# Kernel optimization log

Measured on AMD Instinct MI355X. Metric: run time of the kernel, lower is better.

## Reference

```python
import jax, jax.numpy as jnp
import numpy as np

EMBED_DIM = 1024
HEADS = 16
HEAD_DIM = EMBED_DIM // HEADS


def setup_inputs() -> dict:
    key = jax.random.key(0)
    ks = jax.random.split(key, 5)
    B, N, C = 2, 2048, EMBED_DIM
    scale = 1.0 / np.sqrt(C)
    x = jax.random.normal(ks[0], (B, N, C), dtype=jnp.float32)
    W_qkv = jax.random.normal(ks[1], (C, 3 * C), dtype=jnp.float32) * scale
    b_qkv = jax.random.normal(ks[2], (3 * C,), dtype=jnp.float32) * 0.01
    W_out = jax.random.normal(ks[3], (C, C), dtype=jnp.float32) * scale
    b_out = jax.random.normal(ks[4], (C,), dtype=jnp.float32) * 0.01
    return {"x": x, "W_qkv": W_qkv, "b_qkv": b_qkv, "W_out": W_out, "b_out": b_out}


def reference(x, W_qkv, b_qkv, W_out, b_out):
    B, N, C = x.shape
    qkv = x @ W_qkv + b_qkv                      # [B, N, 3C]
    qkv = qkv.reshape(B, N, 3, HEADS, HEAD_DIM)
    qkv = jnp.transpose(qkv, (2, 0, 3, 1, 4))    # [3, B, H, N, d]
    q, k, v = qkv[0], qkv[1], qkv[2]
    attn = jnp.einsum('bhnd,bhmd->bhnm', q, k) / np.sqrt(HEAD_DIM)
    attn = jax.nn.softmax(attn, axis=-1)
    out = jnp.einsum('bhnm,bhmd->bhnd', attn, v)  # [B, H, N, d]
    out = jnp.transpose(out, (0, 2, 1, 3)).reshape(B, N, C)
    return out @ W_out + b_out
```

## Files before the change

kernel.cpp:

```cpp
#include <hip/hip_runtime.h>
#include <stdint.h>

typedef __bf16 bf16_t;
typedef bf16_t bf16x8 __attribute__((ext_vector_type(8)));
typedef bf16_t bf16x2v __attribute__((ext_vector_type(2)));
typedef float f32x4 __attribute__((ext_vector_type(4)));
typedef float f32x16 __attribute__((ext_vector_type(16)));
typedef uint32_t u32x2 __attribute__((ext_vector_type(2)));
typedef uint32_t u32x4 __attribute__((ext_vector_type(4)));

#define BATCH 2
#define SEQ 2048
#define CDIM 1024
#define NH 16
#define HD 64

#define QSCALE 0.18033688011f

__device__ __forceinline__ uint16_t f32_bf16(float f) {
    __bf16 h = (__bf16)f;
    return __builtin_bit_cast(uint16_t, h);
}

__device__ __forceinline__ uint32_t pack_bf16(float a, float b) {
    bf16x2v t;
    t.x = (__bf16)a;
    t.y = (__bf16)b;
    return __builtin_bit_cast(uint32_t, t);
}

__device__ __forceinline__ bf16x8 ld8(const uint16_t* p) {
    return *reinterpret_cast<const bf16x8*>(p);
}

__device__ __forceinline__ void swap32(uint32_t& a, uint32_t& b) {
#if __has_builtin(__builtin_amdgcn_permlane32_swap)
    u32x2 r = __builtin_amdgcn_permlane32_swap(a, b, false, false);
    a = r.x;
    b = r.y;
#else
    asm("v_permlane32_swap_b32 %0, %1" : "+v"(a), "+v"(b));
#endif
}

__device__ __forceinline__ void gld16(const uint16_t* g, uint16_t* l) {
    __builtin_amdgcn_global_load_lds(
        (__attribute__((address_space(1))) void*)(g),
        (__attribute__((address_space(3))) void*)(l), 16, 0, 0);
}

#define LDS_FENCE() asm volatile("s_waitcnt lgkmcnt(0)" ::: "memory")

__global__ __launch_bounds__(256) void prep_kernel(
        const float* __restrict__ x, uint16_t* __restrict__ x_bf,
        const float* __restrict__ Wqkv, uint16_t* __restrict__ wqkvT,
        const float* __restrict__ Wout, uint16_t* __restrict__ woutT) {
    const int bid = blockIdx.x, tid = threadIdx.x;
    if (bid < 4096) {
        int i = (bid * 256 + tid) * 4;
        float4 v = *(const float4*)(x + i);
        ushort4 o;
        o.x = f32_bf16(v.x);
        o.y = f32_bf16(v.y);
        o.z = f32_bf16(v.z);
        o.w = f32_bf16(v.w);
        *(ushort4*)(x_bf + i) = o;
        return;
    }
    __shared__ float tile[32][33];
    const float* in;
    uint16_t* outp;
    int idx, Cc, ncx;
    if (bid < 4096 + 3072) { idx = bid - 4096; in = Wqkv; outp = wqkvT; Cc = 3072; ncx = 96; }
    else                   { idx = bid - 7168; in = Wout; outp = woutT; Cc = 1024; ncx = 32; }
    const int R = 1024;
    int bx = idx % ncx, by = idx / ncx;
    int c0 = bx * 32, r0 = by * 32;
    int tx = tid & 31, ty = tid >> 5;
#pragma unroll
    for (int i = 0; i < 4; i++)
        tile[ty + i * 8][tx] = in[(size_t)(r0 + ty + i * 8) * Cc + c0 + tx];
    __syncthreads();
    const int rr = tid >> 3, seg = tid & 7;
    ushort4 o;
    o.x = f32_bf16(tile[seg * 4 + 0][rr]);
    o.y = f32_bf16(tile[seg * 4 + 1][rr]);
    o.z = f32_bf16(tile[seg * 4 + 2][rr]);
    o.w = f32_bf16(tile[seg * 4 + 3][rr]);
    *(ushort4*)(outp + (size_t)(c0 + rr) * R + r0 + seg * 4) = o;
}

template <int BM, int BN, int MODE>
__global__ __launch_bounds__(256) void gemm_t(
        const uint16_t* __restrict__ A, const uint16_t* __restrict__ Bt, int K,
        const float* __restrict__ bias,
        uint16_t* __restrict__ qw, uint16_t* __restrict__ kw, uint16_t* __restrict__ vt,
        float* __restrict__ out) {
    constexpr int WT_M = BM / 2, WT_N = BN / 2;
    constexpr int MI = WT_M / 16, NJ = WT_N / 16;
    constexpr int ASEG_W = BM / 64, BSEG_W = BN / 64;
    constexpr int AB = 2 * BM * 32 + 2 * BN * 32;
    constexpr int TS = (MODE == 0) ? 4 * 64 * 68 : 0;
    constexpr int SM = AB > TS ? AB : TS;
    __shared__ uint16_t smem[SM];
    uint16_t* As = smem;
    uint16_t* Bs = smem + 2 * BM * 32;

    const int m0 = blockIdx.y * BM, n0 = blockIdx.x * BN;
    const int tid = threadIdx.x;
    const int w = tid >> 6, lane = tid & 63;
    const int quad = lane >> 4, l16 = lane & 15;
    const int wm = (w >> 1) * WT_M, wn = (w & 1) * WT_N;

    const int srow = lane >> 2;
    const int schunk = (lane & 3) ^ (srow & 3);

    const uint16_t* aP[ASEG_W];
    const uint16_t* bP[BSEG_W];
    int aL[ASEG_W], bL[BSEG_W];
#pragma unroll
    for (int s = 0; s < ASEG_W; s++) {
        int seg = w * ASEG_W + s;
        aP[s] = A + (size_t)(m0 + seg * 16 + srow) * K + schunk * 8;
        aL[s] = seg * 512;
    }
#pragma unroll
    for (int s = 0; s < BSEG_W; s++) {
        int seg = w * BSEG_W + s;
        bP[s] = Bt + (size_t)(n0 + seg * 16 + srow) * K + schunk * 8;
        bL[s] = seg * 512;
    }

    auto stage = [&](int buf, int k0) {
#pragma unroll
        for (int s = 0; s < ASEG_W; s++) gld16(aP[s] + k0, As + buf * BM * 32 + aL[s]);
#pragma unroll
        for (int s = 0; s < BSEG_W; s++) gld16(bP[s] + k0, Bs + buf * BN * 32 + bL[s]);
    };

    const int cslot = (quad ^ (l16 & 3)) * 8;
    f32x4 acc[MI][NJ] = {};

    stage(0, 0);
    const int iters = K / 32;
    for (int it = 0; it < iters; ++it) {
        __syncthreads();
        if (it + 1 < iters) stage((it + 1) & 1, (it + 1) * 32);
        const uint16_t* A_ = As + (it & 1) * BM * 32;
        const uint16_t* B_ = Bs + (it & 1) * BN * 32;
        bf16x8 af[MI], bfr[NJ];
#pragma unroll
        for (int i = 0; i < MI; i++) af[i] = ld8(&A_[(wm + i * 16 + l16) * 32 + cslot]);
#pragma unroll
        for (int j = 0; j < NJ; j++) bfr[j] = ld8(&B_[(wn + j * 16 + l16) * 32 + cslot]);
#pragma unroll
        for (int i = 0; i < MI; i++)
#pragma unroll
            for (int j = 0; j < NJ; j++)
                acc[i][j] = __builtin_amdgcn_mfma_f32_16x16x32_bf16(af[i], bfr[j], acc[i][j], 0, 0, 0);
    }

    const int nbase = n0 + wn;
    float bj[NJ];
#pragma unroll
    for (int j = 0; j < NJ; j++) bj[j] = bias[nbase + j * 16 + l16];

    if constexpr (MODE == 1) {
#pragma unroll
        for (int j = 0; j < NJ; j++) {
#pragma unroll
            for (int i = 0; i < MI; i++)
#pragma unroll
                for (int r = 0; r < 4; r++) {
                    int m = m0 + wm + i * 16 + quad * 4 + r;
                    out[(size_t)m * CDIM + nbase + j * 16 + l16] = acc[i][j][r] + bj[j];
                }
        }
    } else {
        __syncthreads();
        uint16_t* T = smem + w * 64 * 68;
        const int gmb = m0 + wm;
        const int b = gmb >> 11, ns0 = gmb & 2047;
        const int lrow = lane >> 3, lch = lane & 7;

        if (nbase < 2048) {
            const int which = nbase >> 10, h = (nbase & 1023) >> 6;
            const float sc = (which == 0) ? QSCALE : 1.0f;
#pragma unroll
            for (int i = 0; i < 4; i++)
#pragma unroll
                for (int j = 0; j < 4; j++)
#pragma unroll
                    for (int r = 0; r < 4; r++)
                        T[(i * 16 + quad * 4 + r) * 68 + j * 16 + l16] =
                            f32_bf16((acc[i][j][r] + bj[j]) * sc);
            LDS_FENCE();
            uint16_t* dst = ((which == 0) ? qw : kw) +
                            (((size_t)b * NH + h) * SEQ + ns0) * HD;
#pragma unroll
            for (int g = 0; g < 8; g++) {
                int r = g * 8 + lrow;
                bf16x8 v = ld8(&T[r * 68 + lch * 8]);
                *(bf16x8*)(dst + (size_t)r * HD + lch * 8) = v;
            }
        } else {
#pragma unroll
            for (int i = 0; i < 4; i++)
#pragma unroll
                for (int j = 0; j < 4; j++) {
                    u32x2 pr;
                    pr.x = pack_bf16(acc[i][j][0] + bj[j], acc[i][j][1] + bj[j]);
                    pr.y = pack_bf16(acc[i][j][2] + bj[j], acc[i][j][3] + bj[j]);
                    *(u32x2*)&T[(j * 16 + l16) * 68 + i * 16 + quad * 4] = pr;
                }
            LDS_FENCE();
            const int h = (nbase - 2048) >> 6;
            uint16_t* dstb = vt + ((size_t)b * NH + h) * HD * SEQ + ns0;
#pragma unroll
            for (int g = 0; g < 8; g++) {
                int dr = g * 8 + lrow;
                bf16x8 v2 = ld8(&T[dr * 68 + lch * 8]);
                *(bf16x8*)(dstb + (size_t)dr * SEQ + lch * 8) = v2;
            }
        }
    }
}

__global__ __launch_bounds__(256) void attn_kernel(
        const uint16_t* __restrict__ qg, const uint16_t* __restrict__ kg,
        const uint16_t* __restrict__ vt, uint16_t* __restrict__ og) {
    __shared__ uint16_t Ks[2][128 * 64];
    __shared__ uint16_t Vs[2][64 * 128];

    const int bh = blockIdx.x;
    const int qt = blockIdx.y;
    const int tid = threadIdx.x;
    const int w = tid >> 6, lane = tid & 63;
    const int l32 = lane & 31, hi = lane >> 5;
    const int qrow0 = qt * 128 + w * 32;
    const size_t base = (size_t)bh * SEQ * HD;

    bf16x8 qf[4];
#pragma unroll
    for (int s = 0; s < 4; s++)
        qf[s] = ld8(qg + base + (size_t)(qrow0 + l32) * HD + s * 16 + hi * 8);

    const int krow = lane >> 3;
    const int kch = (lane & 7) ^ krow;
    const int vrow = lane >> 4;
    const uint16_t* ksrc[4];
    const uint16_t* vsrc[4];
#pragma unroll
    for (int s = 0; s < 4; s++) {
        int seg = w * 4 + s;
        ksrc[s] = kg + base + (size_t)(seg * 8 + krow) * HD + kch * 8;
        int vd = seg * 4 + vrow;
        int vch = (lane & 15) ^ (vd & 15);
        vsrc[s] = vt + base + (size_t)vd * SEQ + vch * 8;
    }

    f32x16 o_acc[2] = {};
    float l_red = 0.0f;

    auto stage = [&](int buf) {
#pragma unroll
        for (int s = 0; s < 4; s++) {
            int seg = w * 4 + s;
            gld16(ksrc[s], &Ks[buf][seg * 512]);
            ksrc[s] += 128 * HD;
        }
#pragma unroll
        for (int s = 0; s < 4; s++) {
            int seg = w * 4 + s;
            gld16(vsrc[s], &Vs[buf][seg * 512]);
            vsrc[s] += 128;
        }
    };

    stage(0);

    const int kxe = l32 & 7;
    const int vxe = l32 & 15;
    const int krowb = l32 * 64;
    const int vrowb = l32 * 128;
    int kco[4];
#pragma unroll
    for (int s = 0; s < 4; s++) kco[s] = ((2 * s + hi) ^ kxe) * 8;
    int vco[4][2];
#pragma unroll
    for (int kvb = 0; kvb < 4; kvb++)
#pragma unroll
        for (int cp = 0; cp < 2; cp++)
            vco[kvb][cp] = ((kvb * 4 + cp * 2 + hi) ^ vxe) * 8;

    const f32x16 fzero = {};
    const uint16_t* kg_pref = kg + base + (size_t)l32 * HD + hi * 8;

    f32x16 S[2];
    {
        bf16x8 k0[4];
#pragma unroll
        for (int s = 0; s < 4; s++) k0[s] = ld8(kg_pref + s * 16);
        S[0] = fzero;
        __builtin_amdgcn_s_setprio(1);
#pragma unroll
        for (int s = 0; s < 4; s++)
            S[0] = __builtin_amdgcn_mfma_f32_32x32x16_bf16(k0[s], qf[s], S[0], 0, 0, 0);
        __builtin_amdgcn_s_setprio(0);
    }

    const int NT = SEQ / 128;
    for (int it = 0; it < NT; ++it) {
        __syncthreads();
        if (it + 1 < NT) stage((it + 1) & 1);
        const uint16_t* K_ = Ks[it & 1];
        const uint16_t* V_ = Vs[it & 1];
        bf16x8 kf3[4];

#pragma unroll
        for (int kvb = 0; kvb < 4; kvb++) {
            const int cur = kvb & 1, nxt = cur ^ 1;

            bf16x8 kf[4];
            if (kvb < 3) {
#pragma unroll
                for (int s = 0; s < 4; s++)
                    kf[s] = ld8(K_ + (kvb + 1) * 2048 + krowb + kco[s]);
            }
            if (kvb == 2 && it + 1 < NT) {
                const uint16_t* kgp = kg_pref + (size_t)(it + 1) * (128 * HD);
#pragma unroll
                for (int s = 0; s < 4; s++) kf3[s] = ld8(kgp + s * 16);
            }

            bf16x8 vf[2][2];
#pragma unroll
            for (int cp = 0; cp < 2; cp++)
#pragma unroll
                for (int mf = 0; mf < 2; mf++)
                    vf[cp][mf] = ld8(V_ + vrowb + mf * 4096 + vco[kvb][cp]);

            float p[16];
#pragma unroll
            for (int i = 0; i < 16; i++) p[i] = __builtin_amdgcn_exp2f(S[cur][i]);
            {
                float s0 = (p[0] + p[1]) + (p[2] + p[3]);
                float s1 = (p[4] + p[5]) + (p[6] + p[7]);
                float s2 = (p[8] + p[9]) + (p[10] + p[11]);
                float s3 = (p[12] + p[13]) + (p[14] + p[15]);
                l_red += (s0 + s1) + (s2 + s3);
            }
            uint32_t pk0[4], pk1[4];
#pragma unroll
            for (int c = 0; c < 4; c++) {
                pk0[c] = pack_bf16(p[4 * c + 0], p[4 * c + 1]);
                pk1[c] = pack_bf16(p[4 * c + 2], p[4 * c + 3]);
            }

            __builtin_amdgcn_s_setprio(1);
            if (kvb < 3) {
                S[nxt] = fzero;
#pragma unroll
                for (int s = 0; s < 4; s++)
                    S[nxt] = __builtin_amdgcn_mfma_f32_32x32x16_bf16(kf[s], qf[s], S[nxt], 0, 0, 0);
            } else if (it + 1 < NT) {
                S[nxt] = fzero;
#pragma unroll
                for (int s = 0; s < 4; s++)
                    S[nxt] = __builtin_amdgcn_mfma_f32_32x32x16_bf16(kf3[s], qf[s], S[nxt], 0, 0, 0);
            }

#pragma unroll
            for (int cp = 0; cp < 2; cp++) {
                uint32_t b0 = pk0[2 * cp], b2 = pk0[2 * cp + 1];
                uint32_t b1 = pk1[2 * cp], b3 = pk1[2 * cp + 1];
                swap32(b0, b2);
                swap32(b1, b3);
                u32x4 t;
                t.x = b0; t.y = b1; t.z = b2; t.w = b3;
                bf16x8 pb = __builtin_bit_cast(bf16x8, t);
#pragma unroll
                for (int mf = 0; mf < 2; mf++)
                    o_acc[mf] = __builtin_amdgcn_mfma_f32_32x32x16_bf16(vf[cp][mf], pb, o_acc[mf], 0, 0, 0);
            }
            __builtin_amdgcn_s_setprio(0);
        }
    }

    uint32_t la = __builtin_bit_cast(uint32_t, l_red), lb = la;
    swap32(la, lb);
    const float l_tot = __builtin_bit_cast(float, la) + __builtin_bit_cast(float, lb);
    const float inv = __builtin_amdgcn_rcpf(l_tot);

    const int b = bh >> 4, h = bh & 15;
    const int ns = qrow0 + l32;
    uint16_t* orow = og + (((size_t)b * SEQ + ns) * NH + h) * HD;
#pragma unroll
    for (int mf = 0; mf < 2; mf++)
#pragma unroll
        for (int c = 0; c < 4; c++) {
            u32x2 pr;
            pr.x = pack_bf16(o_acc[mf][4 * c + 0] * inv, o_acc[mf][4 * c + 1] * inv);
            pr.y = pack_bf16(o_acc[mf][4 * c + 2] * inv, o_acc[mf][4 * c + 3] * inv);
            *(u32x2*)(orow + mf * 32 + c * 8 + hi * 4) = pr;
        }
}

extern "C" void kernel_launch(void* const* d_in, const int* in_sizes, int n_in,
                              void* d_out, int out_size, void* d_ws, size_t ws_size,
                              hipStream_t stream) {
    const float* x = (const float*)d_in[0];
    const float* Wqkv = (const float*)d_in[1];
    const float* bqkv = (const float*)d_in[2];
    const float* Wout = (const float*)d_in[3];
    const float* bout = (const float*)d_in[4];
    float* out = (float*)d_out;

    uint16_t* ws = (uint16_t*)d_ws;
    uint16_t* x_bf  = ws;
    uint16_t* wqkvT = x_bf + 4194304;
    uint16_t* woutT = wqkvT + 3145728;
    uint16_t* qw    = woutT + 1048576;
    uint16_t* kw    = qw + 4194304;
    uint16_t* vtw   = kw + 4194304;
    uint16_t* attn  = vtw + 4194304;

    prep_kernel<<<8192, 256, 0, stream>>>(x, x_bf, Wqkv, wqkvT, Wout, woutT);

    gemm_t<128, 128, 0><<<dim3(24, 32), 256, 0, stream>>>(
        x_bf, wqkvT, 1024, bqkv, qw, kw, vtw, nullptr);

    attn_kernel<<<dim3(32, 16), 256, 0, stream>>>(qw, kw, vtw, attn);

    gemm_t<64, 128, 1><<<dim3(8, 64), 256, 0, stream>>>(
        attn, woutT, 1024, bout, nullptr, nullptr, nullptr, out);
}
```

Before: 186.9 us.

## Stagger per-wave KV block order and read next K from LDS after partial DMA wait

```diff
diff --git a/kernel.cpp b/kernel.cpp
--- a/kernel.cpp
+++ b/kernel.cpp
@@ -50,6 +50,10 @@
 }
 
 #define LDS_FENCE() asm volatile("s_waitcnt lgkmcnt(0)" ::: "memory")
+#define WAIT_K_DMA() do { \
+    asm volatile("s_waitcnt vmcnt(4)" ::: "memory"); \
+    __builtin_amdgcn_sched_barrier(0); \
+} while (0)
 
 __global__ __launch_bounds__(256) void prep_kernel(
         const float* __restrict__ x, uint16_t* __restrict__ x_bf,
@@ -294,19 +298,18 @@
             vco[kvb][cp] = ((kvb * 4 + cp * 2 + hi) ^ vxe) * 8;
 
     const f32x16 fzero = {};
-    const uint16_t* kg_pref = kg + base + (size_t)l32 * HD + hi * 8;
+    const int wbase = w * 2048;
 
     f32x16 S[2];
+    WAIT_K_DMA();
     {
         bf16x8 k0[4];
 #pragma unroll
-        for (int s = 0; s < 4; s++) k0[s] = ld8(kg_pref + s * 16);
+        for (int s = 0; s < 4; s++) k0[s] = ld8(&Ks[0][wbase] + krowb + kco[s]);
         S[0] = fzero;
-        __builtin_amdgcn_s_setprio(1);
 #pragma unroll
         for (int s = 0; s < 4; s++)
             S[0] = __builtin_amdgcn_mfma_f32_32x32x16_bf16(k0[s], qf[s], S[0], 0, 0, 0);
-        __builtin_amdgcn_s_setprio(0);
     }
 
     const int NT = SEQ / 128;
@@ -315,22 +318,24 @@
         if (it + 1 < NT) stage((it + 1) & 1);
         const uint16_t* K_ = Ks[it & 1];
         const uint16_t* V_ = Vs[it & 1];
-        bf16x8 kf3[4];
-
-#pragma unroll
-        for (int kvb = 0; kvb < 4; kvb++) {
-            const int cur = kvb & 1, nxt = cur ^ 1;
+
+#pragma unroll
+        for (int ph = 0; ph < 4; ph++) {
+            const int cur = ph & 1, nxt = cur ^ 1;
+            const int kvb = (w + ph) & 3;
+            const bool have_next = (ph < 3) || (it + 1 < NT);
 
             bf16x8 kf[4];
-            if (kvb < 3) {
+            if (ph < 3) {
+                const int kvbn = (w + ph + 1) & 3;
 #pragma unroll
                 for (int s = 0; s < 4; s++)
-                    kf[s] = ld8(K_ + (kvb + 1) * 2048 + krowb + kco[s]);
-            }
-            if (kvb == 2 && it + 1 < NT) {
-                const uint16_t* kgp = kg_pref + (size_t)(it + 1) * (128 * HD);
-#pragma unroll
-                for (int s = 0; s < 4; s++) kf3[s] = ld8(kgp + s * 16);
+                    kf[s] = ld8(K_ + kvbn * 2048 + krowb + kco[s]);
+            } else if (it + 1 < NT) {
+                WAIT_K_DMA();
+#pragma unroll
+                for (int s = 0; s < 4; s++)
+                    kf[s] = ld8(&Ks[(it + 1) & 1][wbase] + krowb + kco[s]);
             }
 
             bf16x8 vf[2][2];
@@ -357,17 +362,11 @@
                 pk1[c] = pack_bf16(p[4 * c + 2], p[4 * c + 3]);
             }
 
-            __builtin_amdgcn_s_setprio(1);
-            if (kvb < 3) {
+            if (have_next) {
                 S[nxt] = fzero;
 #pragma unroll
                 for (int s = 0; s < 4; s++)
                     S[nxt] = __builtin_amdgcn_mfma_f32_32x32x16_bf16(kf[s], qf[s], S[nxt], 0, 0, 0);
-            } else if (it + 1 < NT) {
-                S[nxt] = fzero;
-#pragma unroll
-                for (int s = 0; s < 4; s++)
-                    S[nxt] = __builtin_amdgcn_mfma_f32_32x32x16_bf16(kf3[s], qf[s], S[nxt], 0, 0, 0);
             }
 
 #pragma unroll
@@ -383,7 +382,6 @@
                 for (int mf = 0; mf < 2; mf++)
                     o_acc[mf] = __builtin_amdgcn_mfma_f32_32x32x16_bf16(vf[cp][mf], pb, o_acc[mf], 0, 0, 0);
             }
-            __builtin_amdgcn_s_setprio(0);
         }
     }
 
```

Measured after the change: 178.5 us. 4.5% less time.

## Split attention KV range across two wave groups with LDS merge of partials

Applied to the files above, without the earlier changes.

```diff
diff --git a/kernel.cpp b/kernel.cpp
--- a/kernel.cpp
+++ b/kernel.cpp
@@ -226,18 +226,18 @@
     }
 }
 
-__global__ __launch_bounds__(256) void attn_kernel(
+__global__ __launch_bounds__(512, 4) void attn_kernel(
         const uint16_t* __restrict__ qg, const uint16_t* __restrict__ kg,
         const uint16_t* __restrict__ vt, uint16_t* __restrict__ og) {
-    __shared__ uint16_t Ks[2][128 * 64];
-    __shared__ uint16_t Vs[2][64 * 128];
+    __shared__ uint16_t smem[32768];
 
     const int bh = blockIdx.x;
     const int qt = blockIdx.y;
     const int tid = threadIdx.x;
     const int w = tid >> 6, lane = tid & 63;
+    const int g = w >> 2, wl = w & 3;
     const int l32 = lane & 31, hi = lane >> 5;
-    const int qrow0 = qt * 128 + w * 32;
+    const int qrow0 = qt * 128 + wl * 32;
     const size_t base = (size_t)bh * SEQ * HD;
 
     bf16x8 qf[4];
@@ -245,18 +245,22 @@
     for (int s = 0; s < 4; s++)
         qf[s] = ld8(qg + base + (size_t)(qrow0 + l32) * HD + s * 16 + hi * 8);
 
-    const int krow = lane >> 3;
-    const int kch = (lane & 7) ^ krow;
-    const int vrow = lane >> 4;
-    const uint16_t* ksrc[4];
-    const uint16_t* vsrc[4];
-#pragma unroll
-    for (int s = 0; s < 4; s++) {
-        int seg = w * 4 + s;
-        ksrc[s] = kg + base + (size_t)(seg * 8 + krow) * HD + kch * 8;
-        int vd = seg * 4 + vrow;
-        int vch = (lane & 15) ^ (vd & 15);
-        vsrc[s] = vt + base + (size_t)vd * SEQ + vch * 8;
+    const int srow = lane >> 3;
+    const int sch = (lane & 7) ^ srow;
+    const uint16_t* ksrc[2];
+    const uint16_t* vsrc[2];
+#pragma unroll
+    for (int s = 0; s < 2; s++) {
+        int seg = wl * 2 + s;
+        ksrc[s] = kg + base + (size_t)(g * 1024 + seg * 8 + srow) * HD + sch * 8;
+        vsrc[s] = vt + base + (size_t)(seg * 8 + srow) * SEQ + g * 1024 + sch * 8;
+    }
+    uint16_t* Kb[2];
+    uint16_t* Vb[2];
+#pragma unroll
+    for (int buf = 0; buf < 2; buf++) {
+        Kb[buf] = smem + (g * 2 + buf) * 4096;
+        Vb[buf] = smem + 16384 + (g * 2 + buf) * 4096;
     }
 
     f32x16 o_acc[2] = {};
@@ -264,146 +268,168 @@
 
     auto stage = [&](int buf) {
 #pragma unroll
-        for (int s = 0; s < 4; s++) {
-            int seg = w * 4 + s;
-            gld16(ksrc[s], &Ks[buf][seg * 512]);
-            ksrc[s] += 128 * HD;
-        }
-#pragma unroll
-        for (int s = 0; s < 4; s++) {
-            int seg = w * 4 + s;
-            gld16(vsrc[s], &Vs[buf][seg * 512]);
-            vsrc[s] += 128;
+        for (int s = 0; s < 2; s++) {
+            int seg = wl * 2 + s;
+            gld16(ksrc[s], Kb[buf] + seg * 512);
+            ksrc[s] += 64 * HD;
+        }
+#pragma unroll
+        for (int s = 0; s < 2; s++) {
+            int seg = wl * 2 + s;
+            gld16(vsrc[s], Vb[buf] + seg * 512);
+            vsrc[s] += 64;
         }
     };
 
     stage(0);
 
     const int kxe = l32 & 7;
-    const int vxe = l32 & 15;
     const int krowb = l32 * 64;
-    const int vrowb = l32 * 128;
     int kco[4];
 #pragma unroll
     for (int s = 0; s < 4; s++) kco[s] = ((2 * s + hi) ^ kxe) * 8;
-    int vco[4][2];
-#pragma unroll
-    for (int kvb = 0; kvb < 4; kvb++)
+    int vco[2][2];
+#pragma unroll
+    for (int kvb = 0; kvb < 2; kvb++)
 #pragma unroll
         for (int cp = 0; cp < 2; cp++)
-            vco[kvb][cp] = ((kvb * 4 + cp * 2 + hi) ^ vxe) * 8;
+            vco[kvb][cp] = ((kvb * 4 + cp * 2 + hi) ^ kxe) * 8;
 
     const f32x16 fzero = {};
-    const uint16_t* kg_pref = kg + base + (size_t)l32 * HD + hi * 8;
-
-    f32x16 S[2];
-    {
+
+    for (int it = 0; it < 16; ++it) {
+        __syncthreads();
+        if (it + 1 < 16) stage((it + 1) & 1);
+        const uint16_t* K_ = Kb[it & 1];
+        const uint16_t* V_ = Vb[it & 1];
+
         bf16x8 k0[4];
 #pragma unroll
-        for (int s = 0; s < 4; s++) k0[s] = ld8(kg_pref + s * 16);
-        S[0] = fzero;
-        __builtin_amdgcn_s_setprio(1);
+        for (int s = 0; s < 4; s++) k0[s] = ld8(K_ + krowb + kco[s]);
+        f32x16 S0 = fzero;
 #pragma unroll
         for (int s = 0; s < 4; s++)
-            S[0] = __builtin_amdgcn_mfma_f32_32x32x16_bf16(k0[s], qf[s], S[0], 0, 0, 0);
-        __builtin_amdgcn_s_setprio(0);
-    }
-
-    const int NT = SEQ / 128;
-    for (int it = 0; it < NT; ++it) {
-        __syncthreads();
-        if (it + 1 < NT) stage((it + 1) & 1);
-        const uint16_t* K_ = Ks[it & 1];
-        const uint16_t* V_ = Vs[it & 1];
-        bf16x8 kf3[4];
-
-#pragma unroll
-        for (int kvb = 0; kvb < 4; kvb++) {
-            const int cur = kvb & 1, nxt = cur ^ 1;
-
-            bf16x8 kf[4];
-            if (kvb < 3) {
-#pragma unroll
-                for (int s = 0; s < 4; s++)
-                    kf[s] = ld8(K_ + (kvb + 1) * 2048 + krowb + kco[s]);
-            }
-            if (kvb == 2 && it + 1 < NT) {
-                const uint16_t* kgp = kg_pref + (size_t)(it + 1) * (128 * HD);
-#pragma unroll
-                for (int s = 0; s < 4; s++) kf3[s] = ld8(kgp + s * 16);
-            }
-
-            bf16x8 vf[2][2];
-#pragma unroll
-            for (int cp = 0; cp < 2; cp++)
-#pragma unroll
-                for (int mf = 0; mf < 2; mf++)
-                    vf[cp][mf] = ld8(V_ + vrowb + mf * 4096 + vco[kvb][cp]);
-
-            float p[16];
-#pragma unroll
-            for (int i = 0; i < 16; i++) p[i] = __builtin_amdgcn_exp2f(S[cur][i]);
-            {
-                float s0 = (p[0] + p[1]) + (p[2] + p[3]);
-                float s1 = (p[4] + p[5]) + (p[6] + p[7]);
-                float s2 = (p[8] + p[9]) + (p[10] + p[11]);
-                float s3 = (p[12] + p[13]) + (p[14] + p[15]);
-                l_red += (s0 + s1) + (s2 + s3);
-            }
-            uint32_t pk0[4], pk1[4];
-#pragma unroll
-            for (int c = 0; c < 4; c++) {
-                pk0[c] = pack_bf16(p[4 * c + 0], p[4 * c + 1]);
-                pk1[c] = pack_bf16(p[4 * c + 2], p[4 * c + 3]);
-            }
-
-            __builtin_amdgcn_s_setprio(1);
-            if (kvb < 3) {
-                S[nxt] = fzero;
-#pragma unroll
-                for (int s = 0; s < 4; s++)
-                    S[nxt] = __builtin_amdgcn_mfma_f32_32x32x16_bf16(kf[s], qf[s], S[nxt], 0, 0, 0);
-            } else if (it + 1 < NT) {
-                S[nxt] = fzero;
-#pragma unroll
-                for (int s = 0; s < 4; s++)
-                    S[nxt] = __builtin_amdgcn_mfma_f32_32x32x16_bf16(kf3[s], qf[s], S[nxt], 0, 0, 0);
-            }
-
-#pragma unroll
-            for (int cp = 0; cp < 2; cp++) {
-                uint32_t b0 = pk0[2 * cp], b2 = pk0[2 * cp + 1];
-                uint32_t b1 = pk1[2 * cp], b3 = pk1[2 * cp + 1];
-                swap32(b0, b2);
-                swap32(b1, b3);
-                u32x4 t;
-                t.x = b0; t.y = b1; t.z = b2; t.w = b3;
-                bf16x8 pb = __builtin_bit_cast(bf16x8, t);
-#pragma unroll
-                for (int mf = 0; mf < 2; mf++)
-                    o_acc[mf] = __builtin_amdgcn_mfma_f32_32x32x16_bf16(vf[cp][mf], pb, o_acc[mf], 0, 0, 0);
-            }
-            __builtin_amdgcn_s_setprio(0);
+            S0 = __builtin_amdgcn_mfma_f32_32x32x16_bf16(k0[s], qf[s], S0, 0, 0, 0);
+
+        bf16x8 k1[4];
+#pragma unroll
+        for (int s = 0; s < 4; s++) k1[s] = ld8(K_ + 2048 + krowb + kco[s]);
+        bf16x8 vf0[2][2];
+#pragma unroll
+        for (int cp = 0; cp < 2; cp++)
+#pragma unroll
+            for (int mf = 0; mf < 2; mf++)
+                vf0[cp][mf] = ld8(V_ + krowb + mf * 2048 + vco[0][cp]);
+
+        float p0[16];
+#pragma unroll
+        for (int i = 0; i < 16; i++) p0[i] = __builtin_amdgcn_exp2f(S0[i]);
+        {
+            float s0 = (p0[0] + p0[1]) + (p0[2] + p0[3]);
+            float s1 = (p0[4] + p0[5]) + (p0[6] + p0[7]);
+            float s2 = (p0[8] + p0[9]) + (p0[10] + p0[11]);
+            float s3 = (p0[12] + p0[13]) + (p0[14] + p0[15]);
+            l_red += (s0 + s1) + (s2 + s3);
+        }
+        uint32_t a0[4], a1[4];
+#pragma unroll
+        for (int c = 0; c < 4; c++) {
+            a0[c] = pack_bf16(p0[4 * c + 0], p0[4 * c + 1]);
+            a1[c] = pack_bf16(p0[4 * c + 2], p0[4 * c + 3]);
+        }
+
+        f32x16 S1 = fzero;
+#pragma unroll
+        for (int s = 0; s < 4; s++)
+            S1 = __builtin_amdgcn_mfma_f32_32x32x16_bf16(k1[s], qf[s], S1, 0, 0, 0);
+
+#pragma unroll
+        for (int cp = 0; cp < 2; cp++) {
+            uint32_t b0 = a0[2 * cp], b2 = a0[2 * cp + 1];
+            uint32_t b1 = a1[2 * cp], b3 = a1[2 * cp + 1];
+            swap32(b0, b2);
+            swap32(b1, b3);
+            u32x4 t;
+            t.x = b0; t.y = b1; t.z = b2; t.w = b3;
+            bf16x8 pb = __builtin_bit_cast(bf16x8, t);
+#pragma unroll
+            for (int mf = 0; mf < 2; mf++)
+                o_acc[mf] = __builtin_amdgcn_mfma_f32_32x32x16_bf16(vf0[cp][mf], pb, o_acc[mf], 0, 0, 0);
+        }
+
+        bf16x8 vf1[2][2];
+#pragma unroll
+        for (int cp = 0; cp < 2; cp++)
+#pragma unroll
+            for (int mf = 0; mf < 2; mf++)
+                vf1[cp][mf] = ld8(V_ + krowb + mf * 2048 + vco[1][cp]);
+
+        float p1[16];
+#pragma unroll
+        for (int i = 0; i < 16; i++) p1[i] = __builtin_amdgcn_exp2f(S1[i]);
+        {
+            float s0 = (p1[0] + p1[1]) + (p1[2] + p1[3]);
+            float s1 = (p1[4] + p1[5]) + (p1[6] + p1[7]);
+            float s2 = (p1[8] + p1[9]) + (p1[10] + p1[11]);
+            float s3 = (p1[12] + p1[13]) + (p1[14] + p1[15]);
+            l_red += (s0 + s1) + (s2 + s3);
+        }
+        uint32_t c0[4], c1[4];
+#pragma unroll
+        for (int c = 0; c < 4; c++) {
+            c0[c] = pack_bf16(p1[4 * c + 0], p1[4 * c + 1]);
+            c1[c] = pack_bf16(p1[4 * c + 2], p1[4 * c + 3]);
+        }
+#pragma unroll
+        for (int cp = 0; cp < 2; cp++) {
+            uint32_t b0 = c0[2 * cp], b2 = c0[2 * cp + 1];
+            uint32_t b1 = c1[2 * cp], b3 = c1[2 * cp + 1];
+            swap32(b0, b2);
+            swap32(b1, b3);
+            u32x4 t;
+            t.x = b0; t.y = b1; t.z = b2; t.w = b3;
+            bf16x8 pb = __builtin_bit_cast(bf16x8, t);
+#pragma unroll
+            for (int mf = 0; mf < 2; mf++)
+                o_acc[mf] = __builtin_amdgcn_mfma_f32_32x32x16_bf16(vf1[cp][mf], pb, o_acc[mf], 0, 0, 0);
         }
     }
 
     uint32_t la = __builtin_bit_cast(uint32_t, l_red), lb = la;
     swap32(la, lb);
     const float l_tot = __builtin_bit_cast(float, la) + __builtin_bit_cast(float, lb);
-    const float inv = __builtin_amdgcn_rcpf(l_tot);
-
-    const int b = bh >> 4, h = bh & 15;
-    const int ns = qrow0 + l32;
-    uint16_t* orow = og + (((size_t)b * SEQ + ns) * NH + h) * HD;
-#pragma unroll
-    for (int mf = 0; mf < 2; mf++)
-#pragma unroll
-        for (int c = 0; c < 4; c++) {
-            u32x2 pr;
-            pr.x = pack_bf16(o_acc[mf][4 * c + 0] * inv, o_acc[mf][4 * c + 1] * inv);
-            pr.y = pack_bf16(o_acc[mf][4 * c + 2] * inv, o_acc[mf][4 * c + 3] * inv);
-            *(u32x2*)(orow + mf * 32 + c * 8 + hi * 4) = pr;
-        }
+
+    __syncthreads();
+    float* M = (float*)smem;
+    const int mslot = wl * 64 + lane;
+    if (g == 1) {
+#pragma unroll
+        for (int mf = 0; mf < 2; mf++)
+#pragma unroll
+            for (int k = 0; k < 16; k++)
+                M[(mf * 16 + k) * 256 + mslot] = o_acc[mf][k];
+        M[8192 + mslot] = l_tot;
+    }
+    __syncthreads();
+    if (g == 0) {
+        const float inv = __builtin_amdgcn_rcpf(l_tot + M[8192 + mslot]);
+        const int b = bh >> 4, h = bh & 15;
+        const int ns = qrow0 + l32;
+        uint16_t* orow = og + (((size_t)b * SEQ + ns) * NH + h) * HD;
+#pragma unroll
+        for (int mf = 0; mf < 2; mf++)
+#pragma unroll
+            for (int c = 0; c < 4; c++) {
+                float v0 = (o_acc[mf][4 * c + 0] + M[(mf * 16 + 4 * c + 0) * 256 + mslot]) * inv;
+                float v1 = (o_acc[mf][4 * c + 1] + M[(mf * 16 + 4 * c + 1) * 256 + mslot]) * inv;
+                float v2 = (o_acc[mf][4 * c + 2] + M[(mf * 16 + 4 * c + 2) * 256 + mslot]) * inv;
+                float v3 = (o_acc[mf][4 * c + 3] + M[(mf * 16 + 4 * c + 3) * 256 + mslot]) * inv;
+                u32x2 pr;
+                pr.x = pack_bf16(v0, v1);
+                pr.y = pack_bf16(v2, v3);
+                *(u32x2*)(orow + mf * 32 + c * 8 + hi * 4) = pr;
+            }
+    }
 }
 
 extern "C" void kernel_launch(void* const* d_in, const int* in_sizes, int n_in,
@@ -430,7 +456,7 @@
     gemm_t<128, 128, 0><<<dim3(24, 32), 256, 0, stream>>>(
         x_bf, wqkvT, 1024, bqkv, qw, kw, vtw, nullptr);
 
-    attn_kernel<<<dim3(32, 16), 256, 0, stream>>>(qw, kw, vtw, attn);
+    attn_kernel<<<dim3(32, 16), 512, 0, stream>>>(qw, kw, vtw, attn);
 
     gemm_t<64, 128, 1><<<dim3(8, 64), 256, 0, stream>>>(
         attn, woutT, 1024, bout, nullptr, nullptr, nullptr, out);
```

After: 188.3 us. No clear change (+0.7%).
